# Optimization experiments

Measured on AMD Instinct MI355X. Metric: run time of the kernel, lower is better.

## Reference

```python
import jax, jax.numpy as jnp
import numpy as np

# MANO fingertip / palm prior vertex indices from contact_loss
_F1 = [697,698,699,700,712,713,714,715,737,738,739,740,741,743,744,745,746,748,749,750,753,754,755,756,757,758,759,760,761,762,763,764,765,766,767,768]
_F2 = [46,47,48,49,164,165,166,167,194,195,223,237,238,280,281,298,301,317,320,323,324,325,326,327,328,329,330,331,332,333,340,341,342,343,344,345,346,347,348,349,350,351,352,353,354,355]
_F3 = [356,357,358,359,375,376,386,387,396,397,402,403,413,429,433,434,435,436,437,438,439,440,441,442,443,444,452,453,454,455,456,459,460,461,462,463,464,465,466,467]
_F4 = [468,469,470,471,484,485,486,496,497,506,507,513,514,524,545,546,547,548,549,550,551,552,553,555,563,564,565,566,567,570,572,573,574,575,576,577,578]
_F5 = [580,581,582,583,600,601,602,614,615,624,625,630,631,641,663,664,665,666,667,668,670,672,680,681,682,683,684,686,687,688,689,690,691,692,693,694,695]
_F0 = [73,96,98,99,772,774,775,777]
PRIOR_IDX = np.array(_F1 + _F2 + _F3 + _F4 + _F5 + _F0, dtype=np.int32)

KL_COEF = 0.005
A_W, B_W, C_W, D_W, E_W = 1.0, 0.1, 1000.0, 10.0, 10.0  # init kwargs a..e


def _nn(src, trg):
    """Brute-force 1-NN: src [B,N1,3] -> trg [B,N2,3].
    Returns (sq_dist [B,N1], idx [B,N1], diff src-near [B,N1,3])."""
    d2 = (jnp.sum(src * src, -1)[:, :, None]
          + jnp.sum(trg * trg, -1)[:, None, :]
          - 2.0 * jnp.einsum('bnd,bmd->bnm', src, trg))  # [B,N1,N2]
    idx = jnp.argmin(d2, axis=-1)
    near = jnp.take_along_axis(trg, idx[:, :, None], axis=1)
    diff = src - near
    return jnp.sum(diff * diff, axis=-1), idx, diff


def _p2p_signed(x, y, x_normals):
    """point2point_signed(x, y, x_normals): signed dist y->x, unsigned x->y."""
    _, yidx, y2x = _nn(y, x)  # nearest x for each y
    y_nn_normal = jnp.take_along_axis(x_normals, yidx[:, :, None], axis=1)
    in_out = jnp.sign(jnp.sum(y_nn_normal * y2x, axis=-1))
    y2x_signed = jnp.sqrt(jnp.sum(y2x * y2x, axis=-1)) * in_out  # [B,P2]
    _, _, x2y = _nn(x, y)  # nearest y for each x
    x2y_dist = jnp.sqrt(jnp.sum(x2y * x2y, axis=-1))  # [B,P1]
    return y2x_signed, x2y_dist


def _forward(recon_xyz, gt_xyz, recon_normals, gt_normals, obj_xyz, mean, log_var, v_weights):
    B = recon_xyz.shape[0]
    f32 = recon_xyz.dtype
    # --- CVAE recon (L2) + KLD ---
    recon_loss = jnp.sum((recon_xyz - gt_xyz) ** 2) / B
    kld = -0.5 * jnp.sum(1.0 + log_var - mean ** 2 - jnp.exp(log_var)) / B * 10.0
    # --- obj -> hand NN (squared dists, pytorch3d knn_points convention) ---
    recon_d2, recon_idx, _ = _nn(obj_xyz, recon_xyz)  # [B,3000]
    gt_d2, _, _ = _nn(obj_xyz, gt_xyz)
    # --- contact map from GT NN dist thresholding ---
    cmap = jnp.sqrt(gt_d2) < 0.005  # [B,3000] bool
    # --- contact_loss: obj NN to prior (fingertip/palm) recon verts ---
    prior = recon_xyz[:, PRIOR_IDX, :]
    obj_cd, _, _ = _nn(obj_xyz, prior)
    n_pts = jnp.sum(cmap.astype(f32))
    contact = 3000.0 * jnp.where(n_pts > 0, jnp.sum(obj_cd * cmap) / (B * n_pts), 0.0)
    # --- CMap_consistency_loss ---
    recon_cmap = jnp.sqrt(recon_d2) < 0.005
    consistency = -5.0 * jnp.sum((recon_cmap & cmap).astype(f32)) / (n_pts + 1e-4)
    # --- inter_penetr_loss: interior obj points via NN-normal dot sign ---
    nn_hand = jnp.take_along_axis(recon_xyz, recon_idx[:, :, None], axis=1)
    nn_normal = jnp.take_along_axis(recon_normals, recon_idx[:, :, None], axis=1)
    interior = jnp.sum((nn_hand - obj_xyz) * nn_normal, axis=-1) > 0
    penetr = 100.0 * jnp.sum(recon_d2 * interior) / B
    # --- loss_cnet: signed chamfer consistency ---
    vw2 = v_weights ** (1.0 / 2.5)
    o2h, h2o = _p2p_signed(recon_xyz, obj_xyz, recon_normals)
    o2h_gt, h2o_gt = _p2p_signed(gt_xyz, obj_xyz, gt_normals)
    w_dist = (o2h_gt < 0.01) & (o2h_gt > -0.005)
    w_neg = o2h < 0.0
    w = jnp.where(w_neg, 1.5, jnp.where(w_dist, 1.0, 0.1))
    loss_h = 35.0 * (1.0 - KL_COEF) * jnp.mean(jnp.abs(jnp.abs(h2o) - jnp.abs(h2o_gt)) * vw2)
    loss_o = 30.0 * (1.0 - KL_COEF) * jnp.mean(jnp.abs(o2h - o2h_gt) * w)
    cnet = loss_h + loss_o
    return (A_W * recon_loss + B_W * kld + C_W * penetr
            + D_W * contact + E_W * consistency + cnet)


def setup_inputs() -> dict:
    key = jax.random.key(0)
    ks = jax.random.split(key, 8)
    B, NH, NO, Z = 32, 778, 3000, 64
    s = 0.05  # meter-scale point clouds so contact thresholds (5mm) are meaningful
    def unit(k, shape):
        v = jax.random.normal(k, shape, dtype=jnp.float32)
        return v / jnp.linalg.norm(v, axis=-1, keepdims=True)
    return {
        'recon_xyz': jax.random.normal(ks[0], (B, NH, 3), dtype=jnp.float32) * s,
        'gt_xyz': jax.random.normal(ks[1], (B, NH, 3), dtype=jnp.float32) * s,
        'recon_normals': unit(ks[2], (B, NH, 3)),
        'gt_normals': unit(ks[3], (B, NH, 3)),
        'obj_xyz': jax.random.normal(ks[4], (B, NO, 3), dtype=jnp.float32) * s,
        'mean': jax.random.normal(ks[5], (B, Z), dtype=jnp.float32),
        'log_var': jax.random.normal(ks[6], (B, Z), dtype=jnp.float32) * 0.1,
        'v_weights': jax.random.uniform(ks[7], (NH,), dtype=jnp.float32),
    }


def reference(recon_xyz, gt_xyz, recon_normals, gt_normals, obj_xyz, mean, log_var, v_weights):
    return _forward(recon_xyz, gt_xyz, recon_normals, gt_normals, obj_xyz, mean, log_var, v_weights)
```

## Files before the change

### kernel.cpp

```cpp
#include <hip/hip_runtime.h>
#include <math.h>


#define NB 32
#define NH 778
#define NO 3000
#define NZ 64
#define NP 204

#define P_OBJ 4
#define OBJ_PTS 1024
#define OBJ_TILES 3
#define JS8 8
#define JC8 98
#define HC24 24
#define HCS 125

#define T2 12
#define FIN_OBJ_BLKS (NB * T2)
#define FIN_TAIL_BLKS ((NB * NH + 255) / 256)
#define FIN_BLKS (FIN_OBJ_BLKS + FIN_TAIL_BLKS)

#define NKEY (NB * NO)
#define NHT  (NB * NH)

#define ACC_STRIDE 32
#define ACC_FLOATS 512

typedef unsigned int uint32;

__device__ __constant__ int c_prior[NP] = {
  697,698,699,700,712,713,714,715,737,738,739,740,741,743,744,745,746,748,749,750,
  753,754,755,756,757,758,759,760,761,762,763,764,765,766,767,768,
  46,47,48,49,164,165,166,167,194,195,223,237,238,280,281,298,301,317,320,323,
  324,325,326,327,328,329,330,331,332,333,340,341,342,343,344,345,346,347,348,349,
  350,351,352,353,354,355,
  356,357,358,359,375,376,386,387,396,397,402,403,413,429,433,434,435,436,437,438,
  439,440,441,442,443,444,452,453,454,455,456,459,460,461,462,463,464,465,466,467,
  468,469,470,471,484,485,486,496,497,506,507,513,514,524,545,546,547,548,549,550,
  551,552,553,555,563,564,565,566,567,570,572,573,574,575,576,577,578,
  580,581,582,583,600,601,602,614,615,624,625,630,631,641,663,664,665,666,667,668,
  670,672,680,681,682,683,684,686,687,688,689,690,691,692,693,694,695,
  73,96,98,99,772,774,775,777
};

__device__ __constant__ int c_prior_sorted[NP] = {
  46,47,48,49,73,96,98,99,164,165,166,167,194,
  195,223,237,238,280,281,298,301,317,320,323,324,325,326,327,328,329,330,331,
  332,333,340,341,342,343,344,345,346,347,348,349,350,351,352,353,354,355,356,
  357,358,359,375,376,386,387,
  396,397,402,403,413,429,433,434,435,436,437,438,439,440,441,442,443,444,452,
  453,454,455,456,459,460,461,462,463,464,465,466,467,468,469,470,471,484,485,
  486,496,497,506,507,513,514,524,545,546,547,548,549,550,551,552,553,555,563,
  564,565,566,567,570,572,573,574,575,576,577,578,580,581,582,583,
  600,601,602,614,615,624,625,630,631,641,663,664,665,666,667,668,670,672,680,
  681,682,683,684,686,687,688,689,690,691,692,693,694,695,697,698,699,700,712,
  713,714,715,737,738,739,740,741,743,744,745,746,748,749,750,753,754,755,756,
  757,758,759,760,761,762,763,764,765,766,767,768,772,774,775,777
};
__device__ __constant__ int c_psplit8[9] = {0, 6, 14, 19, 58, 97, 131, 154, 204};

__device__ inline float wave_sum(float v) {
  v += __shfl_down(v, 32);
  v += __shfl_down(v, 16);
  v += __shfl_down(v, 8);
  v += __shfl_down(v, 4);
  v += __shfl_down(v, 2);
  v += __shfl_down(v, 1);
  return v;
}

__device__ __forceinline__ float f_min3(float a, float b, float c) {
  float r;
  asm("v_min3_f32 %0, %1, %2, %3" : "=v"(r) : "v"(a), "v"(b), "v"(c));
  return r;
}
__device__ __forceinline__ float f_packao(float t, int j, uint32 mask) {
  float r;
  asm("v_and_or_b32 %0, %1, %2, %3" : "=v"(r) : "v"(t), "s"(mask), "v"(j));
  return r;
}

__global__ __launch_bounds__(256) void mega1t(
    const float* __restrict__ recon, const float* __restrict__ gt,
    const float* __restrict__ obj,
    float* __restrict__ keyR, float* __restrict__ keyG,
    float* __restrict__ priorK,
    float* __restrict__ minHR, float* __restrict__ minHG,
    float* __restrict__ accs)
{
  const int OBJ_B = NB * OBJ_TILES * JS8;
  const int bid = blockIdx.x;
  const int tid = threadIdx.x;
  const uint32 KMASK = 0xFFFFFC00u;

  if (bid == 0) {
    accs[tid] = 0.0f;
    accs[tid + 256] = 0.0f;
  }

  if (bid < OBJ_B) {
    __shared__ float4 shA[JC8];
    __shared__ float4 shB[JC8];
    const int b     = bid / (OBJ_TILES * JS8);
    const int rem   = bid % (OBJ_TILES * JS8);
    const int tile  = rem / JS8;
    const int split = rem % JS8;
    const int jbase = split * JC8;
    const int jcnt  = (NH - jbase < JC8) ? (NH - jbase) : JC8;

    for (int i = tid; i < jcnt; i += 256) {
      const float* p = recon + ((size_t)b * NH + jbase + i) * 3;
      float x = p[0], y = p[1], z = p[2];
      shA[i] = make_float4(x, y, z, x*x + y*y + z*z);
      const float* q = gt + ((size_t)b * NH + jbase + i) * 3;
      float gx = q[0], gy = q[1], gz = q[2];
      shB[i] = make_float4(gx, gy, gz, gx*gx + gy*gy + gz*gz);
    }
    __syncthreads();

    float nx[P_OBJ], ny[P_OBJ], nz[P_OBJ];
    int ob[P_OBJ]; bool val[P_OBJ];
    #pragma unroll
    for (int m = 0; m < P_OBJ; ++m) {
      int o = tile * OBJ_PTS + m * 256 + tid;
      ob[m] = o; val[m] = (o < NO);
      float x = 0.f, y = 0.f, z = 0.f;
      if (val[m]) {
        const float* op = obj + ((size_t)b * NO + o) * 3;
        x = op[0]; y = op[1]; z = op[2];
      }
      nx[m] = -2.f * x; ny[m] = -2.f * y; nz[m] = -2.f * z;
    }

    float bR[P_OBJ], bG[P_OBJ];
    #pragma unroll
    for (int m = 0; m < P_OBJ; ++m) { bR[m] = 3.4e38f; bG[m] = 3.4e38f; }

#define RSTEP(hh0, hh1, jj0, jj1) \
    { _Pragma("unroll") for (int m = 0; m < P_OBJ; ++m) { \
        float t0 = fmaf(nx[m], hh0.x, hh0.w); t0 = fmaf(ny[m], hh0.y, t0); t0 = fmaf(nz[m], hh0.z, t0); \
        float t1 = fmaf(nx[m], hh1.x, hh1.w); t1 = fmaf(ny[m], hh1.y, t1); t1 = fmaf(nz[m], hh1.z, t1); \
        bR[m] = f_min3(bR[m], f_packao(t0, jj0, KMASK), f_packao(t1, jj1, KMASK)); } }
#define GSTEP(gg0, gg1, jj0, jj1) \
    { _Pragma("unroll") for (int m = 0; m < P_OBJ; ++m) { \
        float u0 = fmaf(nx[m], gg0.x, gg0.w); u0 = fmaf(ny[m], gg0.y, u0); u0 = fmaf(nz[m], gg0.z, u0); \
        float u1 = fmaf(nx[m], gg1.x, gg1.w); u1 = fmaf(ny[m], gg1.y, u1); u1 = fmaf(nz[m], gg1.z, u1); \
        bG[m] = f_min3(bG[m], f_packao(u0, jj0, KMASK), f_packao(u1, jj1, KMASK)); } }

    float4 h0 = shA[0], h1 = shA[1];
    int i = 0;
    for (; i + 3 < jcnt; i += 2) {
      float4 g0 = shB[i], g1 = shB[i + 1];
      RSTEP(h0, h1, jbase + i, jbase + i + 1);
      float4 hn0 = shA[i + 2], hn1 = shA[i + 3];
      GSTEP(g0, g1, jbase + i, jbase + i + 1);
      h0 = hn0; h1 = hn1;
    }
    {
      float4 g0 = shB[i], g1 = shB[i + 1];
      RSTEP(h0, h1, jbase + i, jbase + i + 1);
      GSTEP(g0, g1, jbase + i, jbase + i + 1);
      i += 2;
    }
    for (; i < jcnt; ++i) {
      float4 hh = shA[i], gg = shB[i];
      #pragma unroll
      for (int m = 0; m < P_OBJ; ++m) {
        float t0 = fmaf(nx[m], hh.x, hh.w); t0 = fmaf(ny[m], hh.y, t0); t0 = fmaf(nz[m], hh.z, t0);
        bR[m] = fminf(bR[m], f_packao(t0, jbase + i, KMASK));
        float u0 = fmaf(nx[m], gg.x, gg.w); u0 = fmaf(ny[m], gg.y, u0); u0 = fmaf(nz[m], gg.z, u0);
        bG[m] = fminf(bG[m], f_packao(u0, jbase + i, KMASK));
      }
    }
#undef RSTEP
#undef GSTEP

    float bP[P_OBJ];
    #pragma unroll
    for (int m = 0; m < P_OBJ; ++m) bP[m] = 3.4e38f;
    const int pk0 = c_psplit8[split], pk1 = c_psplit8[split + 1];
    int k = pk0;
    for (; k + 1 < pk1; k += 2) {
      float4 ha = shA[c_prior_sorted[k] - jbase];
      float4 hb = shA[c_prior_sorted[k + 1] - jbase];
      #pragma unroll
      for (int m = 0; m < P_OBJ; ++m) {
        float t = fmaf(nx[m], ha.x, ha.w); t = fmaf(ny[m], ha.y, t); t = fmaf(nz[m], ha.z, t);
        float u = fmaf(nx[m], hb.x, hb.w); u = fmaf(ny[m], hb.y, u); u = fmaf(nz[m], hb.z, u);
        bP[m] = f_min3(bP[m], t, u);
      }
    }
    if (k < pk1) {
      float4 ha = shA[c_prior_sorted[k] - jbase];
      #pragma unroll
      for (int m = 0; m < P_OBJ; ++m) {
        float t = fmaf(nx[m], ha.x, ha.w); t = fmaf(ny[m], ha.y, t); t = fmaf(nz[m], ha.z, t);
        bP[m] = fminf(bP[m], t);
      }
    }

    #pragma unroll
    for (int m = 0; m < P_OBJ; ++m) {
      if (!val[m]) continue;
      const size_t idx = (size_t)split * NKEY + (size_t)b * NO + ob[m];
      keyR[idx] = bR[m];
      keyG[idx] = bG[m];
      priorK[idx] = bP[m];
    }
  } else {
    __shared__ float4 sO[HCS];
    const int bid2 = bid - OBJ_B;
    const int oc = bid2 % HC24;
    const int b  = bid2 / HC24;

    const float* Ob = obj + ((size_t)b * NO + oc * HCS) * 3;
    for (int i2 = tid; i2 < HCS; i2 += 256) {
      float x = Ob[3*i2], y = Ob[3*i2+1], z = Ob[3*i2+2];
      sO[i2] = make_float4(x, y, z, x*x + y*y + z*z);
    }
    __syncthreads();

    float nrx[3], nry[3], nrz[3];
    float ngx[3], ngy[3], ngz[3];
    #pragma unroll
    for (int m = 0; m < 3; ++m) {
      const int j = m * 256 + tid;
      const float* rp = recon + ((size_t)b * NH + j) * 3;
      const float* gp = gt    + ((size_t)b * NH + j) * 3;
      nrx[m] = -2.f*rp[0]; nry[m] = -2.f*rp[1]; nrz[m] = -2.f*rp[2];
      ngx[m] = -2.f*gp[0]; ngy[m] = -2.f*gp[1]; ngz[m] = -2.f*gp[2];
    }

    float mR[3], mG[3];
    #pragma unroll
    for (int m = 0; m < 3; ++m) { mR[m] = 3.4e38f; mG[m] = 3.4e38f; }

#define HSTEP(oo0, oo1) \
    { _Pragma("unroll") for (int m = 0; m < 3; ++m) { \
        float t0 = fmaf(nrx[m], oo0.x, oo0.w); t0 = fmaf(nry[m], oo0.y, t0); t0 = fmaf(nrz[m], oo0.z, t0); \
        float t1 = fmaf(nrx[m], oo1.x, oo1.w); t1 = fmaf(nry[m], oo1.y, t1); t1 = fmaf(nrz[m], oo1.z, t1); \
        mR[m] = f_min3(mR[m], t0, t1); \
        float u0 = fmaf(ngx[m], oo0.x, oo0.w); u0 = fmaf(ngy[m], oo0.y, u0); u0 = fmaf(ngz[m], oo0.z, u0); \
        float u1 = fmaf(ngx[m], oo1.x, oo1.w); u1 = fmaf(ngy[m], oo1.y, u1); u1 = fmaf(ngz[m], oo1.z, u1); \
        mG[m] = f_min3(mG[m], u0, u1); } }

    float4 o0 = sO[0], o1 = sO[1];
    int k2 = 0;
    for (; k2 + 3 < HCS; k2 += 2) {
      float4 a0 = sO[k2 + 2], a1 = sO[k2 + 3];
      HSTEP(o0, o1);
      o0 = a0; o1 = a1;
    }
    HSTEP(o0, o1);
    k2 += 2;
    for (; k2 < HCS; ++k2) {
      float4 oc4 = sO[k2];
      #pragma unroll
      for (int m = 0; m < 3; ++m) {
        float t0 = fmaf(nrx[m], oc4.x, oc4.w); t0 = fmaf(nry[m], oc4.y, t0); t0 = fmaf(nrz[m], oc4.z, t0);
        mR[m] = fminf(mR[m], t0);
        float u0 = fmaf(ngx[m], oc4.x, oc4.w); u0 = fmaf(ngy[m], oc4.y, u0); u0 = fmaf(ngz[m], oc4.z, u0);
        mG[m] = fminf(mG[m], u0);
      }
    }
#undef HSTEP

    #pragma unroll
    for (int m = 0; m < 3; ++m) {
      const int j = m * 256 + tid;
      const size_t idx = (size_t)oc * NHT + (size_t)b * NH + j;
      minHR[idx] = mR[m];
      minHG[idx] = mG[m];
    }

    const int tw = bid2 & 3;
    if ((tid >> 6) == tw) {
      const int j3 = 768 + (tid & 63);
      const bool v3 = (j3 < NH);
      float rx=0.f,ry=0.f,rz=0.f,gx=0.f,gy=0.f,gz=0.f;
      if (v3) {
        const float* rp = recon + ((size_t)b * NH + j3) * 3;
        const float* gp = gt    + ((size_t)b * NH + j3) * 3;
        rx=rp[0];ry=rp[1];rz=rp[2]; gx=gp[0];gy=gp[1];gz=gp[2];
      }
      const float n3rx=-2.f*rx, n3ry=-2.f*ry, n3rz=-2.f*rz;
      const float n3gx=-2.f*gx, n3gy=-2.f*gy, n3gz=-2.f*gz;
      float m3R = 3.4e38f, m3G = 3.4e38f;
      int k3 = 0;
      for (; k3 + 1 < HCS; k3 += 2) {
        float4 q0 = sO[k3], q1 = sO[k3 + 1];
        float t0 = fmaf(n3rx, q0.x, q0.w); t0 = fmaf(n3ry, q0.y, t0); t0 = fmaf(n3rz, q0.z, t0);
        float t1 = fmaf(n3rx, q1.x, q1.w); t1 = fmaf(n3ry, q1.y, t1); t1 = fmaf(n3rz, q1.z, t1);
        m3R = f_min3(m3R, t0, t1);
        float u0 = fmaf(n3gx, q0.x, q0.w); u0 = fmaf(n3gy, q0.y, u0); u0 = fmaf(n3gz, q0.z, u0);
        float u1 = fmaf(n3gx, q1.x, q1.w); u1 = fmaf(n3gy, q1.y, u1); u1 = fmaf(n3gz, q1.z, u1);
        m3G = f_min3(m3G, u0, u1);
      }
      {
        float4 q0 = sO[HCS - 1];
        float t0 = fmaf(n3rx, q0.x, q0.w); t0 = fmaf(n3ry, q0.y, t0); t0 = fmaf(n3rz, q0.z, t0);
        m3R = fminf(m3R, t0);
        float u0 = fmaf(n3gx, q0.x, q0.w); u0 = fmaf(n3gy, q0.y, u0); u0 = fmaf(n3gz, q0.z, u0);
        m3G = fminf(m3G, u0);
      }
      if (v3) {
        const size_t idx = (size_t)oc * NHT + (size_t)b * NH + j3;
        minHR[idx] = m3R;
        minHG[idx] = m3G;
      }
    }
  }
}

__global__ __launch_bounds__(256) void mega2n(
    const float* __restrict__ recon, const float* __restrict__ gt,
    const float* __restrict__ rnorm, const float* __restrict__ gnorm,
    const float* __restrict__ obj,
    const float* __restrict__ mean, const float* __restrict__ logv,
    const float* __restrict__ vw,
    const float* __restrict__ keyR, const float* __restrict__ keyG,
    const float* __restrict__ priorK,
    const float* __restrict__ minHR, const float* __restrict__ minHG,
    float* __restrict__ accs)
{
  __shared__ float red[4][5];
  const int bid = blockIdx.x;
  const int tid = threadIdx.x;
  const int lane = tid & 63, wv = tid >> 6;

  if (bid < FIN_OBJ_BLKS) {
    const int b = bid / T2;
    const int tile = bid % T2;
    const int o = tile * 256 + tid;
    float penetr = 0.f, nptsv = 0.f, contactv = 0.f, consistv = 0.f, lossov = 0.f;
    if (o < NO) {
      const float* op = obj + ((size_t)b * NO + o) * 3;
      const float ox = op[0], oy = op[1], oz = op[2];
      const float o2 = ox*ox + oy*oy + oz*oz;
      const size_t base = (size_t)b * NO + o;

      float kR = 3.4e38f, kG = 3.4e38f, bP = 3.4e38f;
      #pragma unroll
      for (int s = 0; s < JS8; ++s) {
        kR = fminf(kR, keyR[(size_t)s * NKEY + base]);
        kG = fminf(kG, keyG[(size_t)s * NKEY + base]);
        bP = fminf(bP, priorK[(size_t)s * NKEY + base]);
      }
      uint32 kRb = __float_as_uint(kR), kGb = __float_as_uint(kG);
      int idxR = (int)(kRb & 0x3FFu), idxG = (int)(kGb & 0x3FFu);
      float d2R = fmaxf(__uint_as_float(kRb & 0xFFFFFC00u) + o2, 0.f);
      float d2G = fmaxf(__uint_as_float(kGb & 0xFFFFFC00u) + o2, 0.f);
      float d2P = fmaxf(bP + o2, 0.f);

      const float* hR = recon + ((size_t)b * NH + idxR) * 3;
      const float* nR = rnorm + ((size_t)b * NH + idxR) * 3;
      float dotR = (ox - hR[0]) * nR[0] + (oy - hR[1]) * nR[1] + (oz - hR[2]) * nR[2];
      const float* hG = gt + ((size_t)b * NH + idxG) * 3;
      const float* nG = gnorm + ((size_t)b * NH + idxG) * 3;
      float dotG = (ox - hG[0]) * nG[0] + (oy - hG[1]) * nG[1] + (oz - hG[2]) * nG[2];

      float sgnR = (dotR > 0.f) ? 1.f : ((dotR < 0.f) ? -1.f : 0.f);
      float sgnG = (dotG > 0.f) ? 1.f : ((dotG < 0.f) ? -1.f : 0.f);
      float sR_ = sqrtf(d2R), sG_ = sqrtf(d2G);
      float o2h = sR_ * sgnR, o2hg = sG_ * sgnG;

      bool interior = dotR < 0.f;
      bool cmap = sG_ < 0.005f;
      bool rcmap = sR_ < 0.005f;

      penetr   = interior ? d2R : 0.f;
      nptsv    = cmap ? 1.f : 0.f;
      contactv = cmap ? d2P : 0.f;
      consistv = (cmap && rcmap) ? 1.f : 0.f;
      float w = (o2h < 0.f) ? 1.5f
              : (((o2hg < 0.01f) && (o2hg > -0.005f)) ? 1.f : 0.1f);
      lossov = fabsf(o2h - o2hg) * w;
    }

    float vals[5] = {penetr, nptsv, contactv, consistv, lossov};
    #pragma unroll
    for (int q = 0; q < 5; ++q) {
      float s = wave_sum(vals[q]);
      if (lane == 0) red[wv][q] = s;
    }
    __syncthreads();
    if (tid < 5) {
      float s = red[0][tid] + red[1][tid] + red[2][tid] + red[3][tid];
      atomicAdd(&accs[tid * ACC_STRIDE], s);
    }
  } else {
    const int t = (bid - FIN_OBJ_BLKS) * 256 + tid;
    float lossh = 0.f, rsum = 0.f, ksum = 0.f;
    if (t < NB * NH) {
      const float* rp = recon + (size_t)t * 3;
      const float* gp = gt + (size_t)t * 3;
      float rx = rp[0], ry = rp[1], rz = rp[2];
      float gx = gp[0], gy = gp[1], gz = gp[2];
      float d0 = rx - gx, d1 = ry - gy, d2 = rz - gz;
      rsum = d0*d0 + d1*d1 + d2*d2;

      float mRt = 3.4e38f, mGt = 3.4e38f;
      #pragma unroll
      for (int c = 0; c < HC24; ++c) {
        mRt = fminf(mRt, minHR[(size_t)c * NHT + t]);
        mGt = fminf(mGt, minHG[(size_t)c * NHT + t]);
      }
      float r2 = rx*rx + ry*ry + rz*rz;
      float g2 = gx*gx + gy*gy + gz*gz;
      float d2Rh = fmaxf(mRt + r2, 0.f);
      float d2Gh = fmaxf(mGt + g2, 0.f);
      int j = t % NH;
      lossh = fabsf(sqrtf(d2Rh) - sqrtf(d2Gh)) * powf(vw[j], 0.4f);
    }
    if (t < NB * NZ) {
      float m = mean[t], lv = logv[t];
      ksum = 1.f + lv - m * m - expf(lv);
    }
    float vals[3] = {lossh, rsum, ksum};
    #pragma unroll
    for (int q = 0; q < 3; ++q) {
      float s = wave_sum(vals[q]);
      if (lane == 0) red[wv][q] = s;
    }
    __syncthreads();
    if (tid < 3) {
      float s = red[0][tid] + red[1][tid] + red[2][tid] + red[3][tid];
      atomicAdd(&accs[(5 + tid) * ACC_STRIDE], s);
    }
  }
}

__global__ void final_fb(const float* __restrict__ a, float* __restrict__ out) {
  const float recon_loss = a[6 * ACC_STRIDE] / (float)NB;
  const float kld = -0.5f * a[7 * ACC_STRIDE] / (float)NB * 10.f;
  const float penetr = 100.f * a[0] / (float)NB;
  const float npts = a[1 * ACC_STRIDE];
  const float contact = (npts > 0.f) ? (3000.f * a[2 * ACC_STRIDE] / ((float)NB * npts)) : 0.f;
  const float consistency = -5.f * a[3 * ACC_STRIDE] / (npts + 0.0001f);
  const float lossh = 35.f * (1.f - 0.005f) * (a[5 * ACC_STRIDE] / (float)(NB * NH));
  const float losso = 30.f * (1.f - 0.005f) * (a[4 * ACC_STRIDE] / (float)(NB * NO));
  out[0] = recon_loss + 0.1f*kld + 1000.f*penetr + 10.f*contact + 10.f*consistency + lossh + losso;
}

__global__ __launch_bounds__(256) void obj_mono(
    const float* __restrict__ recon, const float* __restrict__ gt,
    const float* __restrict__ rnorm, const float* __restrict__ gnorm,
    const float* __restrict__ obj, float* __restrict__ accs)
{
  __shared__ float4 sR[NH];
  __shared__ float4 sG[NH];
  __shared__ float red[4][5];
  const int b = blockIdx.x / 12;
  const int tile = blockIdx.x % 12;
  const int tid = threadIdx.x;
  for (int i = tid; i < NH; i += 256) {
    const float* p = recon + ((size_t)b * NH + i) * 3;
    float x = p[0], y = p[1], z = p[2];
    sR[i] = make_float4(x, y, z, x*x + y*y + z*z);
    const float* q = gt + ((size_t)b * NH + i) * 3;
    float gx = q[0], gy = q[1], gz = q[2];
    sG[i] = make_float4(gx, gy, gz, gx*gx + gy*gy + gz*gz);
  }
  __syncthreads();
  const int o = tile * 256 + tid;
  float penetr = 0.f, nptsv = 0.f, contactv = 0.f, consistv = 0.f, lossov = 0.f;
  if (o < NO) {
    const float* op = obj + ((size_t)b * NO + o) * 3;
    const float ox = op[0], oy = op[1], oz = op[2];
    const float nx = -2.f*ox, ny = -2.f*oy, nz = -2.f*oz;
    const float o2 = ox*ox + oy*oy + oz*oz;
    float bR = 3.4e38f, bG = 3.4e38f; int iR = 0, iG = 0;
    for (int i = 0; i < NH; ++i) {
      float4 h = sR[i];
      float t = fmaf(nx, h.x, h.w); t = fmaf(ny, h.y, t); t = fmaf(nz, h.z, t);
      if (t < bR) { bR = t; iR = i; }
      float4 g = sG[i];
      float u = fmaf(nx, g.x, g.w); u = fmaf(ny, g.y, u); u = fmaf(nz, g.z, u);
      if (u < bG) { bG = u; iG = i; }
    }
    float bP = 3.4e38f;
    for (int k = 0; k < NP; ++k) {
      float4 h = sR[c_prior[k]];
      float t = fmaf(nx, h.x, h.w); t = fmaf(ny, h.y, t); t = fmaf(nz, h.z, t);
      bP = fminf(bP, t);
    }
    float d2R = fmaxf(bR + o2, 0.f);
    float d2G = fmaxf(bG + o2, 0.f);
    float d2P = fmaxf(bP + o2, 0.f);
    float4 hR = sR[iR];
    const float* nR = rnorm + ((size_t)b * NH + iR) * 3;
    float dotR = (ox-hR.x)*nR[0] + (oy-hR.y)*nR[1] + (oz-hR.z)*nR[2];
    float4 hG = sG[iG];
    const float* nG = gnorm + ((size_t)b * NH + iG) * 3;
    float dotG = (ox-hG.x)*nG[0] + (oy-hG.y)*nG[1] + (oz-hG.z)*nG[2];
    float sgnR = (dotR > 0.f) ? 1.f : ((dotR < 0.f) ? -1.f : 0.f);
    float sgnG = (dotG > 0.f) ? 1.f : ((dotG < 0.f) ? -1.f : 0.f);
    float sR_ = sqrtf(d2R), sG_ = sqrtf(d2G);
    float o2h = sR_*sgnR, o2hg = sG_*sgnG;
    bool interior = dotR < 0.f;
    bool cmap = sG_ < 0.005f, rcmap = sR_ < 0.005f;
    penetr = interior ? d2R : 0.f;
    nptsv = cmap ? 1.f : 0.f;
    contactv = cmap ? d2P : 0.f;
    consistv = (cmap && rcmap) ? 1.f : 0.f;
    float w = (o2h < 0.f) ? 1.5f : (((o2hg < 0.01f) && (o2hg > -0.005f)) ? 1.f : 0.1f);
    lossov = fabsf(o2h - o2hg) * w;
  }
  float vals[5] = {penetr, nptsv, contactv, consistv, lossov};
  const int lane = tid & 63, wv = tid >> 6;
  for (int q = 0; q < 5; ++q) {
    float s = wave_sum(vals[q]);
    if (lane == 0) red[wv][q] = s;
  }
  __syncthreads();
  if (tid < 5) {
    float s = red[0][tid] + red[1][tid] + red[2][tid] + red[3][tid];
    atomicAdd(&accs[tid * ACC_STRIDE], s);
  }
}

__global__ __launch_bounds__(256) void hand_full(
    const float* __restrict__ recon, const float* __restrict__ gt,
    const float* __restrict__ obj, const float* __restrict__ vw,
    float* __restrict__ accs)
{
  __shared__ float4 sO[500];
  __shared__ float red[4];
  const int b = blockIdx.x >> 2;
  const int j = ((blockIdx.x & 3) << 8) + threadIdx.x;
  const bool valid = j < NH;
  float rx=0,ry=0,rz=0,gx=0,gy=0,gz=0;
  if (valid) {
    const float* rp = recon + ((size_t)b * NH + j) * 3;
    const float* gp = gt + ((size_t)b * NH + j) * 3;
    rx=rp[0];ry=rp[1];rz=rp[2]; gx=gp[0];gy=gp[1];gz=gp[2];
  }
  const float nrx=-2.f*rx, nry=-2.f*ry, nrz=-2.f*rz;
  const float ngx=-2.f*gx, ngy=-2.f*gy, ngz=-2.f*gz;
  const float r2 = rx*rx+ry*ry+rz*rz, g2 = gx*gx+gy*gy+gz*gz;
  float mR = 3.4e38f, mG = 3.4e38f;
  for (int oc = 0; oc < 6; ++oc) {
    __syncthreads();
    const float* Ob = obj + ((size_t)b * NO + oc * 500) * 3;
    for (int i = threadIdx.x; i < 500; i += 256) {
      float x = Ob[3*i], y = Ob[3*i+1], z = Ob[3*i+2];
      sO[i] = make_float4(x, y, z, x*x + y*y + z*z);
    }
    __syncthreads();
    if (valid) {
      for (int k = 0; k < 500; ++k) {
        float4 o4 = sO[k];
        float t = fmaf(nrx,o4.x,o4.w); t = fmaf(nry,o4.y,t); t = fmaf(nrz,o4.z,t);
        mR = fminf(mR, t);
        float u = fmaf(ngx,o4.x,o4.w); u = fmaf(ngy,o4.y,u); u = fmaf(ngz,o4.z,u);
        mG = fminf(mG, u);
      }
    }
  }
  float lossh = valid ? fabsf(sqrtf(fmaxf(mR+r2,0.f)) - sqrtf(fmaxf(mG+g2,0.f))) * powf(vw[j], 0.4f) : 0.f;
  const int lane = threadIdx.x & 63, wv = threadIdx.x >> 6;
  float s = wave_sum(lossh);
  if (lane == 0) red[wv] = s;
  __syncthreads();
  if (threadIdx.x == 0) atomicAdd(&accs[5 * ACC_STRIDE], red[0]+red[1]+red[2]+red[3]);
}

__global__ __launch_bounds__(256) void tail_nomins(
    const float* __restrict__ recon, const float* __restrict__ gt,
    const float* __restrict__ mean, const float* __restrict__ logv,
    float* __restrict__ accs)
{
  __shared__ float red[4][2];
  const int t = blockIdx.x * 256 + threadIdx.x;
  float rsum = 0.f, ksum = 0.f;
  if (t < NB * NH) {
    const float* rp = recon + (size_t)t * 3;
    const float* gp = gt + (size_t)t * 3;
    float d0 = rp[0]-gp[0], d1 = rp[1]-gp[1], d2 = rp[2]-gp[2];
    rsum = d0*d0 + d1*d1 + d2*d2;
  }
  if (t < NB * NZ) {
    float m = mean[t], lv = logv[t];
    ksum = 1.f + lv - m*m - expf(lv);
  }
  float vals[2] = {rsum, ksum};
  const int lane = threadIdx.x & 63, wv = threadIdx.x >> 6;
  for (int q = 0; q < 2; ++q) {
    float s = wave_sum(vals[q]);
    if (lane == 0) red[wv][q] = s;
  }
  __syncthreads();
  if (threadIdx.x < 2) {
    float s = red[0][threadIdx.x] + red[1][threadIdx.x] + red[2][threadIdx.x] + red[3][threadIdx.x];
    atomicAdd(&accs[(6 + threadIdx.x) * ACC_STRIDE], s);
  }
}

__global__ void init_small(float* accs) {
  int t = threadIdx.x;
  accs[t] = 0.0f;
  accs[t + 256] = 0.0f;
}

extern "C" void kernel_launch(void* const* d_in, const int* in_sizes, int n_in,
                              void* d_out, int out_size, void* d_ws, size_t ws_size,
                              hipStream_t stream) {
  const float* recon = (const float*)d_in[0];
  const float* gt    = (const float*)d_in[1];
  const float* rnorm = (const float*)d_in[2];
  const float* gnorm = (const float*)d_in[3];
  const float* obj   = (const float*)d_in[4];
  const float* mean  = (const float*)d_in[5];
  const float* logv  = (const float*)d_in[6];
  const float* vw    = (const float*)d_in[7];
  float* out = (float*)d_out;

  float* accs = (float*)d_ws;
  float* base = (float*)((char*)d_ws + ACC_FLOATS * sizeof(float));

  const size_t needed = ACC_FLOATS * sizeof(float)
                      + (3ull * JS8 * NKEY + 2ull * HC24 * NHT) * sizeof(float);

  if (ws_size >= needed) {
    float* keyR   = base;
    float* keyG   = keyR + (size_t)JS8 * NKEY;
    float* priorK = keyG + (size_t)JS8 * NKEY;
    float* minHR  = priorK + (size_t)JS8 * NKEY;
    float* minHG  = minHR + (size_t)HC24 * NHT;
    const int g1 = NB * OBJ_TILES * JS8 + NB * HC24;
    mega1t<<<g1, 256, 0, stream>>>(
        recon, gt, obj, keyR, keyG, priorK, minHR, minHG, accs);
    mega2n<<<FIN_BLKS, 256, 0, stream>>>(
        recon, gt, rnorm, gnorm, obj, mean, logv, vw,
        keyR, keyG, priorK, minHR, minHG, accs);
    final_fb<<<1, 1, 0, stream>>>(accs, out);
  } else {
    init_small<<<1, 256, 0, stream>>>(accs);
    obj_mono<<<NB * 12, 256, 0, stream>>>(recon, gt, rnorm, gnorm, obj, accs);
    hand_full<<<NB * 4, 256, 0, stream>>>(recon, gt, obj, vw, accs);
    tail_nomins<<<(NB * NH + 255) / 256, 256, 0, stream>>>(recon, gt, mean, logv, accs);
    final_fb<<<1, 1, 0, stream>>>(accs, out);
  }
}
```

Before: 115.6 us.

## Halve split counts, use single-wave finisher blocks and striped atomic accumulators

Cuts the hand-vertex splits for object tiles from 8 to 4 and the object chunks for hand minima from 24 to 12. Each first-stage block now does twice the work, and the second stage reads half as many partial-min arrays. The second-stage kernel now uses 64-thread single-wave blocks that skip shared-memory reduction and barriers. Atomics are spread across 32 cache-line-separated slots per quantity, and the final kernel sums those slots. The trade-off is fewer, longer first-stage blocks, which lowers parallelism against less partial-result traffic and less atomic contention.

```diff
diff --git a/kernel.cpp b/kernel.cpp
--- a/kernel.cpp
+++ b/kernel.cpp
@@ -11,21 +11,20 @@
 #define P_OBJ 4
 #define OBJ_PTS 1024
 #define OBJ_TILES 3
-#define JS8 8
-#define JC8 98
-#define HC24 24
-#define HCS 125
-
-#define T2 12
-#define FIN_OBJ_BLKS (NB * T2)
-#define FIN_TAIL_BLKS ((NB * NH + 255) / 256)
-#define FIN_BLKS (FIN_OBJ_BLKS + FIN_TAIL_BLKS)
+#define JS4 4
+#define JC4 195
+#define HC12 12
+#define HCS12 250
 
 #define NKEY (NB * NO)
 #define NHT  (NB * NH)
 
-#define ACC_STRIDE 32
-#define ACC_FLOATS 512
+#define M2_OBJ_BLKS (NB * 47)
+#define M2_TAIL_BLKS (NB * NH / 64)
+#define M2_BLKS (M2_OBJ_BLKS + M2_TAIL_BLKS)
+
+#define ACCIDX(q, s) ((((q) * 32) + (s)) * 32)
+#define ACC_FLOATS (9 * 32 * 32)
 
 typedef unsigned int uint32;
 
@@ -58,7 +57,7 @@
   713,714,715,737,738,739,740,741,743,744,745,746,748,749,750,753,754,755,756,
   757,758,759,760,761,762,763,764,765,766,767,768,772,774,775,777
 };
-__device__ __constant__ int c_psplit8[9] = {0, 6, 14, 19, 58, 97, 131, 154, 204};
+__device__ __constant__ int c_psplit4[5] = {0, 13, 58, 131, 204};
 
 __device__ inline float wave_sum(float v) {
   v += __shfl_down(v, 32);
@@ -89,25 +88,24 @@
     float* __restrict__ minHR, float* __restrict__ minHG,
     float* __restrict__ accs)
 {
-  const int OBJ_B = NB * OBJ_TILES * JS8;
+  const int OBJ_B = NB * OBJ_TILES * JS4;
   const int bid = blockIdx.x;
   const int tid = threadIdx.x;
   const uint32 KMASK = 0xFFFFFC00u;
 
   if (bid == 0) {
-    accs[tid] = 0.0f;
-    accs[tid + 256] = 0.0f;
+    for (int i = tid; i < ACC_FLOATS; i += 256) accs[i] = 0.0f;
   }
 
   if (bid < OBJ_B) {
-    __shared__ float4 shA[JC8];
-    __shared__ float4 shB[JC8];
-    const int b     = bid / (OBJ_TILES * JS8);
-    const int rem   = bid % (OBJ_TILES * JS8);
-    const int tile  = rem / JS8;
-    const int split = rem % JS8;
-    const int jbase = split * JC8;
-    const int jcnt  = (NH - jbase < JC8) ? (NH - jbase) : JC8;
+    __shared__ float4 shA[JC4];
+    __shared__ float4 shB[JC4];
+    const int b     = bid / (OBJ_TILES * JS4);
+    const int rem   = bid % (OBJ_TILES * JS4);
+    const int tile  = rem / JS4;
+    const int split = rem % JS4;
+    const int jbase = split * JC4;
+    const int jcnt  = (NH - jbase < JC4) ? (NH - jbase) : JC4;
 
     for (int i = tid; i < jcnt; i += 256) {
       const float* p = recon + ((size_t)b * NH + jbase + i) * 3;
@@ -179,7 +177,7 @@
     float bP[P_OBJ];
     #pragma unroll
     for (int m = 0; m < P_OBJ; ++m) bP[m] = 3.4e38f;
-    const int pk0 = c_psplit8[split], pk1 = c_psplit8[split + 1];
+    const int pk0 = c_psplit4[split], pk1 = c_psplit4[split + 1];
     int k = pk0;
     for (; k + 1 < pk1; k += 2) {
       float4 ha = shA[c_prior_sorted[k] - jbase];
@@ -209,13 +207,13 @@
       priorK[idx] = bP[m];
     }
   } else {
-    __shared__ float4 sO[HCS];
+    __shared__ float4 sO[HCS12];
     const int bid2 = bid - OBJ_B;
-    const int oc = bid2 % HC24;
-    const int b  = bid2 / HC24;
-
-    const float* Ob = obj + ((size_t)b * NO + oc * HCS) * 3;
-    for (int i2 = tid; i2 < HCS; i2 += 256) {
+    const int oc = bid2 % HC12;
+    const int b  = bid2 / HC12;
+
+    const float* Ob = obj + ((size_t)b * NO + oc * HCS12) * 3;
+    for (int i2 = tid; i2 < HCS12; i2 += 256) {
       float x = Ob[3*i2], y = Ob[3*i2+1], z = Ob[3*i2+2];
       sO[i2] = make_float4(x, y, z, x*x + y*y + z*z);
     }
@@ -247,14 +245,14 @@
 
     float4 o0 = sO[0], o1 = sO[1];
     int k2 = 0;
-    for (; k2 + 3 < HCS; k2 += 2) {
+    for (; k2 + 3 < HCS12; k2 += 2) {
       float4 a0 = sO[k2 + 2], a1 = sO[k2 + 3];
       HSTEP(o0, o1);
       o0 = a0; o1 = a1;
     }
     HSTEP(o0, o1);
     k2 += 2;
-    for (; k2 < HCS; ++k2) {
+    for (; k2 < HCS12; ++k2) {
       float4 oc4 = sO[k2];
       #pragma unroll
       for (int m = 0; m < 3; ++m) {
@@ -288,7 +286,7 @@
       const float n3gx=-2.f*gx, n3gy=-2.f*gy, n3gz=-2.f*gz;
       float m3R = 3.4e38f, m3G = 3.4e38f;
       int k3 = 0;
-      for (; k3 + 1 < HCS; k3 += 2) {
+      for (; k3 + 1 < HCS12; k3 += 2) {
         float4 q0 = sO[k3], q1 = sO[k3 + 1];
         float t0 = fmaf(n3rx, q0.x, q0.w); t0 = fmaf(n3ry, q0.y, t0); t0 = fmaf(n3rz, q0.z, t0);
         float t1 = fmaf(n3rx, q1.x, q1.w); t1 = fmaf(n3ry, q1.y, t1); t1 = fmaf(n3rz, q1.z, t1);
@@ -297,8 +295,8 @@
         float u1 = fmaf(n3gx, q1.x, q1.w); u1 = fmaf(n3gy, q1.y, u1); u1 = fmaf(n3gz, q1.z, u1);
         m3G = f_min3(m3G, u0, u1);
       }
-      {
-        float4 q0 = sO[HCS - 1];
+      if (HCS12 & 1) {
+        float4 q0 = sO[HCS12 - 1];
         float t0 = fmaf(n3rx, q0.x, q0.w); t0 = fmaf(n3ry, q0.y, t0); t0 = fmaf(n3rz, q0.z, t0);
         m3R = fminf(m3R, t0);
         float u0 = fmaf(n3gx, q0.x, q0.w); u0 = fmaf(n3gy, q0.y, u0); u0 = fmaf(n3gz, q0.z, u0);
@@ -313,7 +311,7 @@
   }
 }
 
-__global__ __launch_bounds__(256) void mega2n(
+__global__ __launch_bounds__(64) void mega2s(
     const float* __restrict__ recon, const float* __restrict__ gt,
     const float* __restrict__ rnorm, const float* __restrict__ gnorm,
     const float* __restrict__ obj,
@@ -324,15 +322,13 @@
     const float* __restrict__ minHR, const float* __restrict__ minHG,
     float* __restrict__ accs)
 {
-  __shared__ float red[4][5];
   const int bid = blockIdx.x;
   const int tid = threadIdx.x;
-  const int lane = tid & 63, wv = tid >> 6;
-
-  if (bid < FIN_OBJ_BLKS) {
-    const int b = bid / T2;
-    const int tile = bid % T2;
-    const int o = tile * 256 + tid;
+  const int line = bid & 31;
+
+  if (bid < M2_OBJ_BLKS) {
+    const int b = bid / 47;
+    const int o = (bid % 47) * 64 + tid;
     float penetr = 0.f, nptsv = 0.f, contactv = 0.f, consistv = 0.f, lossov = 0.f;
     if (o < NO) {
       const float* op = obj + ((size_t)b * NO + o) * 3;
@@ -342,7 +338,7 @@
 
       float kR = 3.4e38f, kG = 3.4e38f, bP = 3.4e38f;
       #pragma unroll
-      for (int s = 0; s < JS8; ++s) {
+      for (int s = 0; s < JS4; ++s) {
         kR = fminf(kR, keyR[(size_t)s * NKEY + base]);
         kG = fminf(kG, keyG[(size_t)s * NKEY + base]);
         bP = fminf(bP, priorK[(size_t)s * NKEY + base]);
@@ -382,17 +378,12 @@
     #pragma unroll
     for (int q = 0; q < 5; ++q) {
       float s = wave_sum(vals[q]);
-      if (lane == 0) red[wv][q] = s;
-    }
-    __syncthreads();
-    if (tid < 5) {
-      float s = red[0][tid] + red[1][tid] + red[2][tid] + red[3][tid];
-      atomicAdd(&accs[tid * ACC_STRIDE], s);
+      if (tid == 0) atomicAdd(&accs[ACCIDX(q, line)], s);
     }
   } else {
-    const int t = (bid - FIN_OBJ_BLKS) * 256 + tid;
+    const int t = (bid - M2_OBJ_BLKS) * 64 + tid;
     float lossh = 0.f, rsum = 0.f, ksum = 0.f;
-    if (t < NB * NH) {
+    {
       const float* rp = recon + (size_t)t * 3;
       const float* gp = gt + (size_t)t * 3;
       float rx = rp[0], ry = rp[1], rz = rp[2];
@@ -402,7 +393,7 @@
 
       float mRt = 3.4e38f, mGt = 3.4e38f;
       #pragma unroll
-      for (int c = 0; c < HC24; ++c) {
+      for (int c = 0; c < HC12; ++c) {
         mRt = fminf(mRt, minHR[(size_t)c * NHT + t]);
         mGt = fminf(mGt, minHG[(size_t)c * NHT + t]);
       }
@@ -421,26 +412,32 @@
     #pragma unroll
     for (int q = 0; q < 3; ++q) {
       float s = wave_sum(vals[q]);
-      if (lane == 0) red[wv][q] = s;
-    }
-    __syncthreads();
-    if (tid < 3) {
-      float s = red[0][tid] + red[1][tid] + red[2][tid] + red[3][tid];
-      atomicAdd(&accs[(5 + tid) * ACC_STRIDE], s);
+      if (tid == 0) atomicAdd(&accs[ACCIDX(5 + q, line)], s);
     }
   }
 }
 
 __global__ void final_fb(const float* __restrict__ a, float* __restrict__ out) {
-  const float recon_loss = a[6 * ACC_STRIDE] / (float)NB;
-  const float kld = -0.5f * a[7 * ACC_STRIDE] / (float)NB * 10.f;
-  const float penetr = 100.f * a[0] / (float)NB;
-  const float npts = a[1 * ACC_STRIDE];
-  const float contact = (npts > 0.f) ? (3000.f * a[2 * ACC_STRIDE] / ((float)NB * npts)) : 0.f;
-  const float consistency = -5.f * a[3 * ACC_STRIDE] / (npts + 0.0001f);
-  const float lossh = 35.f * (1.f - 0.005f) * (a[5 * ACC_STRIDE] / (float)(NB * NH));
-  const float losso = 30.f * (1.f - 0.005f) * (a[4 * ACC_STRIDE] / (float)(NB * NO));
-  out[0] = recon_loss + 0.1f*kld + 1000.f*penetr + 10.f*contact + 10.f*consistency + lossh + losso;
+  __shared__ float sums[8];
+  const int q = threadIdx.x;
+  if (q < 8) {
+    float s = 0.f;
+    for (int l = 0; l < 32; ++l) s += a[ACCIDX(q, l)];
+    sums[q] = s;
+  }
+  __syncthreads();
+  if (threadIdx.x == 0) {
+    const float recon_loss = sums[6] / (float)NB;
+    const float kld = -0.5f * sums[7] / (float)NB * 10.f;
+    const float penetr = 100.f * sums[0] / (float)NB;
+    const float npts = sums[1];
+    const float contact = (npts > 0.f) ? (3000.f * sums[2] / ((float)NB * npts)) : 0.f;
+    const float consistency = -5.f * sums[3] / (npts + 0.0001f);
+    const float lossh = 35.f * (1.f - 0.005f) * (sums[5] / (float)(NB * NH));
+    const float losso = 30.f * (1.f - 0.005f) * (sums[4] / (float)(NB * NO));
+    out[0] = recon_loss + 0.1f * kld + 1000.f * penetr + 10.f * contact
+           + 10.f * consistency + lossh + losso;
+  }
 }
 
 __global__ __launch_bounds__(256) void obj_mono(
@@ -516,7 +513,7 @@
   __syncthreads();
   if (tid < 5) {
     float s = red[0][tid] + red[1][tid] + red[2][tid] + red[3][tid];
-    atomicAdd(&accs[tid * ACC_STRIDE], s);
+    atomicAdd(&accs[ACCIDX(tid, blockIdx.x & 31)], s);
   }
 }
 
@@ -563,7 +560,7 @@
   float s = wave_sum(lossh);
   if (lane == 0) red[wv] = s;
   __syncthreads();
-  if (threadIdx.x == 0) atomicAdd(&accs[5 * ACC_STRIDE], red[0]+red[1]+red[2]+red[3]);
+  if (threadIdx.x == 0) atomicAdd(&accs[ACCIDX(5, blockIdx.x & 31)], red[0]+red[1]+red[2]+red[3]);
 }
 
 __global__ __launch_bounds__(256) void tail_nomins(
@@ -593,14 +590,12 @@
   __syncthreads();
   if (threadIdx.x < 2) {
     float s = red[0][threadIdx.x] + red[1][threadIdx.x] + red[2][threadIdx.x] + red[3][threadIdx.x];
-    atomicAdd(&accs[(6 + threadIdx.x) * ACC_STRIDE], s);
+    atomicAdd(&accs[ACCIDX(6 + threadIdx.x, blockIdx.x & 31)], s);
   }
 }
 
 __global__ void init_small(float* accs) {
-  int t = threadIdx.x;
-  accs[t] = 0.0f;
-  accs[t + 256] = 0.0f;
+  for (int i = threadIdx.x; i < ACC_FLOATS; i += 256) accs[i] = 0.0f;
 }
 
 extern "C" void kernel_launch(void* const* d_in, const int* in_sizes, int n_in,
@@ -620,26 +615,26 @@
   float* base = (float*)((char*)d_ws + ACC_FLOATS * sizeof(float));
 
   const size_t needed = ACC_FLOATS * sizeof(float)
-                      + (3ull * JS8 * NKEY + 2ull * HC24 * NHT) * sizeof(float);
+                      + (3ull * JS4 * NKEY + 2ull * HC12 * NHT) * sizeof(float);
 
   if (ws_size >= needed) {
     float* keyR   = base;
-    float* keyG   = keyR + (size_t)JS8 * NKEY;
-    float* priorK = keyG + (size_t)JS8 * NKEY;
-    float* minHR  = priorK + (size_t)JS8 * NKEY;
-    float* minHG  = minHR + (size_t)HC24 * NHT;
-    const int g1 = NB * OBJ_TILES * JS8 + NB * HC24;
+    float* keyG   = keyR + (size_t)JS4 * NKEY;
+    float* priorK = keyG + (size_t)JS4 * NKEY;
+    float* minHR  = priorK + (size_t)JS4 * NKEY;
+    float* minHG  = minHR + (size_t)HC12 * NHT;
+    const int g1 = NB * OBJ_TILES * JS4 + NB * HC12;
     mega1t<<<g1, 256, 0, stream>>>(
         recon, gt, obj, keyR, keyG, priorK, minHR, minHG, accs);
-    mega2n<<<FIN_BLKS, 256, 0, stream>>>(
+    mega2s<<<M2_BLKS, 64, 0, stream>>>(
         recon, gt, rnorm, gnorm, obj, mean, logv, vw,
         keyR, keyG, priorK, minHR, minHG, accs);
-    final_fb<<<1, 1, 0, stream>>>(accs, out);
+    final_fb<<<1, 64, 0, stream>>>(accs, out);
   } else {
     init_small<<<1, 256, 0, stream>>>(accs);
     obj_mono<<<NB * 12, 256, 0, stream>>>(recon, gt, rnorm, gnorm, obj, accs);
     hand_full<<<NB * 4, 256, 0, stream>>>(recon, gt, obj, vw, accs);
     tail_nomins<<<(NB * NH + 255) / 256, 256, 0, stream>>>(recon, gt, mean, logv, accs);
-    final_fb<<<1, 1, 0, stream>>>(accs, out);
-  }
-}
+    final_fb<<<1, 64, 0, stream>>>(accs, out);
+  }
+}
```

After: 108.7 us (median of 2 runs). 1.06x faster.
